# Kernel tuning notes

Hardware: AMD Instinct MI355X
Metric: run time of the kernel (lower is better)

## Reference

```python
import jax, jax.numpy as jnp
import numpy as np

def setup_inputs() -> dict:
    key = jax.random.key(0)
    k1, k2, k3 = jax.random.split(key, 3)
    B, N, Din, Dout = 4, 1024, 64, 64
    x = jax.random.normal(k1, (B, N, Din), dtype=jnp.float32)
    # nn.Linear(2*Din, Dout): weight [Dout, 2*Din], bias [Dout]
    W = jax.random.normal(k2, (Dout, 2 * Din), dtype=jnp.float32) * (1.0 / np.sqrt(2 * Din))
    b = jax.random.normal(k3, (Dout,), dtype=jnp.float32) * 0.01
    return {"x": x, "W": W, "b": b}

def reference(x, W, b):
    # Faithful to: y_pairs[b,i,j] = Linear(cat([x[b,i], x[b,j]])); y = max_i y_pairs
    # Separable form: cat([x1,x2]) @ W.T = x1 @ W1.T + x2 @ W2.T
    Din = x.shape[-1]
    W1 = W[:, :Din]   # acts on x1 (row index i)
    W2 = W[:, Din:]   # acts on x2 (column index j)
    a = jnp.einsum('bnd,od->bno', x, W1)  # [B, N, Dout], i-contribution
    c = jnp.einsum('bnd,od->bno', x, W2)  # [B, N, Dout], j-contribution
    y_pairs = a[:, :, None, :] + c[:, None, :, :] + b  # [B, i, j, Dout]
    return jnp.max(y_pairs, axis=1)  # pool over i (dim=-3) -> [B, N, Dout]
```

## Files before the change

### kernel.cpp

```cpp
#include <hip/hip_runtime.h>

#define NB 4
#define NN 1024
#define DK 64
#define DO 64
#define CHUNKS 64
#define RPC 16
#define WPAD 68
#define XPAD 68

__global__ __launch_bounds__(256) void pe_k1(const float* __restrict__ x,
                                             const float* __restrict__ W,
                                             float* __restrict__ out,
                                             float* __restrict__ wsmax) {
    __shared__ float Wt[128 * WPAD];
    __shared__ float xs[RPC * XPAD];
    __shared__ float red[16 * 64];

    const int t  = threadIdx.x;
    const int bi = blockIdx.x;
    const int b  = bi >> 6;
    const int ch = bi & 63;
    const int m0 = ch * RPC;

    const float4* W4 = (const float4*)W;
    #pragma unroll
    for (int i = 0; i < 8; ++i) {
        int g4 = t + 256 * i;
        float4 wv = W4[g4];
        int base = g4 * 4;
        int o = base >> 7;
        int k = base & 127;
        Wt[(k + 0) * WPAD + o] = wv.x;
        Wt[(k + 1) * WPAD + o] = wv.y;
        Wt[(k + 2) * WPAD + o] = wv.z;
        Wt[(k + 3) * WPAD + o] = wv.w;
    }
    {
        const float4* x4 = (const float4*)(x + ((size_t)b * NN + m0) * DK);
        float4 xv = x4[t];
        int base = t * 4;
        int r = base >> 6;
        int d = base & 63;
        *(float4*)&xs[r * XPAD + d] = xv;
    }
    __syncthreads();

    const int og = t & 15;
    const int r  = t >> 4;

    float4 aa = make_float4(0.f, 0.f, 0.f, 0.f);
    float4 cc = make_float4(0.f, 0.f, 0.f, 0.f);
    const float* xr = &xs[r * XPAD];

    #pragma unroll
    for (int d = 0; d < 64; d += 4) {
        float4 xq = *(const float4*)&xr[d];
        float xv[4] = {xq.x, xq.y, xq.z, xq.w};
        #pragma unroll
        for (int j = 0; j < 4; ++j) {
            float xs_ = xv[j];
            float4 w1 = *(const float4*)&Wt[(d + j) * WPAD + og * 4];
            float4 w2 = *(const float4*)&Wt[(64 + d + j) * WPAD + og * 4];
            aa.x += xs_ * w1.x; aa.y += xs_ * w1.y; aa.z += xs_ * w1.z; aa.w += xs_ * w1.w;
            cc.x += xs_ * w2.x; cc.y += xs_ * w2.y; cc.z += xs_ * w2.z; cc.w += xs_ * w2.w;
        }
    }

    {
        size_t oidx = (((size_t)b * NN) + (m0 + r)) * DO + og * 4;
        *(float4*)&out[oidx] = cc;
    }

    *(float4*)&red[r * 64 + og * 4] = aa;
    __syncthreads();
    if (t < 64) {
        float v = red[t];
        #pragma unroll
        for (int rr = 1; rr < 16; ++rr) v = fmaxf(v, red[rr * 64 + t]);
        wsmax[((size_t)b * CHUNKS + ch) * 64 + t] = v;
    }
}

__global__ __launch_bounds__(256) void pe_k2(const float* __restrict__ bias,
                                             const float* __restrict__ wsmax,
                                             float* __restrict__ out) {
    __shared__ float addv[64];
    const int t  = threadIdx.x;
    const int bi = blockIdx.x;
    const int b  = bi >> 6;
    const int rb = bi & 63;

    if (t < 64) {
        const float* wp = wsmax + (size_t)b * CHUNKS * 64 + t;
        float v = wp[0];
        #pragma unroll
        for (int ch = 1; ch < CHUNKS; ++ch) v = fmaxf(v, wp[ch * 64]);
        addv[t] = v + bias[t];
    }
    __syncthreads();

    size_t base = ((size_t)b * NN + rb * 16) * DO;
    float4* o4 = (float4*)(out + base);
    float4 val = o4[t];
    int oc = (t & 15) * 4;
    val.x += addv[oc + 0];
    val.y += addv[oc + 1];
    val.z += addv[oc + 2];
    val.w += addv[oc + 3];
    o4[t] = val;
}

extern "C" void kernel_launch(void* const* d_in, const int* in_sizes, int n_in,
                              void* d_out, int out_size, void* d_ws, size_t ws_size,
                              hipStream_t stream) {
    const float* x    = (const float*)d_in[0];
    const float* W    = (const float*)d_in[1];
    const float* bias = (const float*)d_in[2];
    float* out   = (float*)d_out;
    float* wsmax = (float*)d_ws;

    pe_k1<<<NB * CHUNKS, 256, 0, stream>>>(x, W, out, wsmax);
    pe_k2<<<NB * 64, 256, 0, stream>>>(bias, wsmax, out);
}
```

Before: 12.66 us.

## Recompute c-projection in second kernel instead of round-tripping through output

The first kernel now computes only the i-side projection and its per-chunk max, and no longer writes the c-projection to the output buffer. The second kernel loads x and the other half of W, recomputes the c-projection, adds the reduced max plus bias, and writes the output once. This removes a global write and re-read of the full output and halves the shared-memory weight staging per kernel. In exchange x is read twice, and the cross-chunk max reduction is split over all 256 threads instead of 64.

```diff
diff --git a/kernel.cpp b/kernel.cpp
--- a/kernel.cpp
+++ b/kernel.cpp
@@ -1,114 +1,132 @@
 #include <hip/hip_runtime.h>
 
-#define NB 4
-#define NN 1024
-#define DK 64
-#define DO 64
-#define CHUNKS 64
-#define RPC 16
 #define WPAD 68
-#define XPAD 68
 
 __global__ __launch_bounds__(256) void pe_k1(const float* __restrict__ x,
                                              const float* __restrict__ W,
-                                             float* __restrict__ out,
                                              float* __restrict__ wsmax) {
-    __shared__ float Wt[128 * WPAD];
-    __shared__ float xs[RPC * XPAD];
+    __shared__ float Wt[64 * WPAD];
+    __shared__ float xs[16 * WPAD];
     __shared__ float red[16 * 64];
 
     const int t  = threadIdx.x;
-    const int bi = blockIdx.x;
-    const int b  = bi >> 6;
-    const int ch = bi & 63;
-    const int m0 = ch * RPC;
+    const int b  = blockIdx.x >> 6;
+    const int ch = blockIdx.x & 63;
+    const int m0 = ch << 4;
 
     const float4* W4 = (const float4*)W;
     #pragma unroll
-    for (int i = 0; i < 8; ++i) {
-        int g4 = t + 256 * i;
-        float4 wv = W4[g4];
-        int base = g4 * 4;
-        int o = base >> 7;
-        int k = base & 127;
-        Wt[(k + 0) * WPAD + o] = wv.x;
-        Wt[(k + 1) * WPAD + o] = wv.y;
-        Wt[(k + 2) * WPAD + o] = wv.z;
-        Wt[(k + 3) * WPAD + o] = wv.w;
+    for (int i = 0; i < 4; ++i) {
+        int id = t + 256 * i;
+        int o = id >> 4, q = id & 15;
+        float4 wv = W4[o * 32 + q];
+        Wt[(4 * q + 0) * WPAD + o] = wv.x;
+        Wt[(4 * q + 1) * WPAD + o] = wv.y;
+        Wt[(4 * q + 2) * WPAD + o] = wv.z;
+        Wt[(4 * q + 3) * WPAD + o] = wv.w;
     }
     {
-        const float4* x4 = (const float4*)(x + ((size_t)b * NN + m0) * DK);
+        const float4* x4 = (const float4*)(x + ((size_t)b * 1024 + m0) * 64);
         float4 xv = x4[t];
-        int base = t * 4;
-        int r = base >> 6;
-        int d = base & 63;
-        *(float4*)&xs[r * XPAD + d] = xv;
+        *(float4*)&xs[(t >> 4) * WPAD + 4 * (t & 15)] = xv;
     }
     __syncthreads();
 
+    const int r  = t >> 4;
     const int og = t & 15;
-    const int r  = t >> 4;
-
-    float4 aa = make_float4(0.f, 0.f, 0.f, 0.f);
-    float4 cc = make_float4(0.f, 0.f, 0.f, 0.f);
-    const float* xr = &xs[r * XPAD];
+    const float* xr = &xs[r * WPAD];
+    float ax = 0.f, ay = 0.f, az = 0.f, aw = 0.f;
 
     #pragma unroll
-    for (int d = 0; d < 64; d += 4) {
-        float4 xq = *(const float4*)&xr[d];
-        float xv[4] = {xq.x, xq.y, xq.z, xq.w};
-        #pragma unroll
-        for (int j = 0; j < 4; ++j) {
-            float xs_ = xv[j];
-            float4 w1 = *(const float4*)&Wt[(d + j) * WPAD + og * 4];
-            float4 w2 = *(const float4*)&Wt[(64 + d + j) * WPAD + og * 4];
-            aa.x += xs_ * w1.x; aa.y += xs_ * w1.y; aa.z += xs_ * w1.z; aa.w += xs_ * w1.w;
-            cc.x += xs_ * w2.x; cc.y += xs_ * w2.y; cc.z += xs_ * w2.z; cc.w += xs_ * w2.w;
-        }
+    for (int q = 0; q < 16; ++q) {
+        float4 xq = *(const float4*)&xr[4 * q];
+        float4 w0 = *(const float4*)&Wt[(4 * q + 0) * WPAD + og * 4];
+        float4 w1 = *(const float4*)&Wt[(4 * q + 1) * WPAD + og * 4];
+        float4 w2 = *(const float4*)&Wt[(4 * q + 2) * WPAD + og * 4];
+        float4 w3 = *(const float4*)&Wt[(4 * q + 3) * WPAD + og * 4];
+        ax += xq.x * w0.x; ay += xq.x * w0.y; az += xq.x * w0.z; aw += xq.x * w0.w;
+        ax += xq.y * w1.x; ay += xq.y * w1.y; az += xq.y * w1.z; aw += xq.y * w1.w;
+        ax += xq.z * w2.x; ay += xq.z * w2.y; az += xq.z * w2.z; aw += xq.z * w2.w;
+        ax += xq.w * w3.x; ay += xq.w * w3.y; az += xq.w * w3.z; aw += xq.w * w3.w;
     }
+    *(float4*)&red[r * 64 + og * 4] = make_float4(ax, ay, az, aw);
+    __syncthreads();
 
-    {
-        size_t oidx = (((size_t)b * NN) + (m0 + r)) * DO + og * 4;
-        *(float4*)&out[oidx] = cc;
-    }
-
-    *(float4*)&red[r * 64 + og * 4] = aa;
-    __syncthreads();
     if (t < 64) {
         float v = red[t];
         #pragma unroll
         for (int rr = 1; rr < 16; ++rr) v = fmaxf(v, red[rr * 64 + t]);
-        wsmax[((size_t)b * CHUNKS + ch) * 64 + t] = v;
+        wsmax[((size_t)(b << 6) + ch) * 64 + t] = v;
     }
 }
 
-__global__ __launch_bounds__(256) void pe_k2(const float* __restrict__ bias,
+__global__ __launch_bounds__(256) void pe_k2(const float* __restrict__ x,
+                                             const float* __restrict__ W,
+                                             const float* __restrict__ bias,
                                              const float* __restrict__ wsmax,
                                              float* __restrict__ out) {
+    __shared__ float Wt[64 * WPAD];
+    __shared__ float xs[16 * WPAD];
+    __shared__ float amx[4 * 64];
     __shared__ float addv[64];
+
     const int t  = threadIdx.x;
-    const int bi = blockIdx.x;
-    const int b  = bi >> 6;
-    const int rb = bi & 63;
+    const int b  = blockIdx.x >> 6;
+    const int ch = blockIdx.x & 63;
+    const int m0 = ch << 4;
 
+    const float4* W4 = (const float4*)W;
+    #pragma unroll
+    for (int i = 0; i < 4; ++i) {
+        int id = t + 256 * i;
+        int o = id >> 4, q = id & 15;
+        float4 wv = W4[o * 32 + 16 + q];
+        Wt[(4 * q + 0) * WPAD + o] = wv.x;
+        Wt[(4 * q + 1) * WPAD + o] = wv.y;
+        Wt[(4 * q + 2) * WPAD + o] = wv.z;
+        Wt[(4 * q + 3) * WPAD + o] = wv.w;
+    }
+    {
+        const float4* x4 = (const float4*)(x + ((size_t)b * 1024 + m0) * 64);
+        float4 xv = x4[t];
+        *(float4*)&xs[(t >> 4) * WPAD + 4 * (t & 15)] = xv;
+    }
+    {
+        const int o = t & 63, g = t >> 6;
+        const float* wp = wsmax + (size_t)b * 4096 + o;
+        float v = wp[(size_t)g * 64];
+        #pragma unroll
+        for (int s = 1; s < 16; ++s) v = fmaxf(v, wp[(size_t)(g + 4 * s) * 64]);
+        amx[g * 64 + o] = v;
+    }
+    __syncthreads();
     if (t < 64) {
-        const float* wp = wsmax + (size_t)b * CHUNKS * 64 + t;
-        float v = wp[0];
-        #pragma unroll
-        for (int ch = 1; ch < CHUNKS; ++ch) v = fmaxf(v, wp[ch * 64]);
+        float v = fmaxf(fmaxf(amx[t], amx[64 + t]), fmaxf(amx[128 + t], amx[192 + t]));
         addv[t] = v + bias[t];
     }
     __syncthreads();
 
-    size_t base = ((size_t)b * NN + rb * 16) * DO;
-    float4* o4 = (float4*)(out + base);
-    float4 val = o4[t];
-    int oc = (t & 15) * 4;
-    val.x += addv[oc + 0];
-    val.y += addv[oc + 1];
-    val.z += addv[oc + 2];
-    val.w += addv[oc + 3];
-    o4[t] = val;
+    const int r  = t >> 4;
+    const int og = t & 15;
+    const float* xr = &xs[r * WPAD];
+    float4 add = *(const float4*)&addv[og * 4];
+    float cx = add.x, cy = add.y, cz = add.z, cw = add.w;
+
+    #pragma unroll
+    for (int q = 0; q < 16; ++q) {
+        float4 xq = *(const float4*)&xr[4 * q];
+        float4 w0 = *(const float4*)&Wt[(4 * q + 0) * WPAD + og * 4];
+        float4 w1 = *(const float4*)&Wt[(4 * q + 1) * WPAD + og * 4];
+        float4 w2 = *(const float4*)&Wt[(4 * q + 2) * WPAD + og * 4];
+        float4 w3 = *(const float4*)&Wt[(4 * q + 3) * WPAD + og * 4];
+        cx += xq.x * w0.x; cy += xq.x * w0.y; cz += xq.x * w0.z; cw += xq.x * w0.w;
+        cx += xq.y * w1.x; cy += xq.y * w1.y; cz += xq.y * w1.z; cw += xq.y * w1.w;
+        cx += xq.z * w2.x; cy += xq.z * w2.y; cz += xq.z * w2.z; cw += xq.z * w2.w;
+        cx += xq.w * w3.x; cy += xq.w * w3.y; cz += xq.w * w3.z; cw += xq.w * w3.w;
+    }
+
+    size_t oidx = ((size_t)b * 1024 + (m0 + r)) * 64 + og * 4;
+    *(float4*)&out[oidx] = make_float4(cx, cy, cz, cw);
 }
 
 extern "C" void kernel_launch(void* const* d_in, const int* in_sizes, int n_in,
@@ -120,6 +138,6 @@
     float* out   = (float*)d_out;
     float* wsmax = (float*)d_ws;
 
-    pe_k1<<<NB * CHUNKS, 256, 0, stream>>>(x, W, out, wsmax);
-    pe_k2<<<NB * 64, 256, 0, stream>>>(bias, wsmax, out);
+    pe_k1<<<4 * 64, 256, 0, stream>>>(x, W, wsmax);
+    pe_k2<<<4 * 64, 256, 0, stream>>>(x, W, bias, wsmax, out);
 }
```

New measurement: 12.82 us (median of 2 runs). About the same (+1.3%).
